# Kernel optimization log

Hardware: AMD Instinct MI355X
Metric: run time of the kernel (lower is better)

Reference implementation:

```python
import jax, jax.numpy as jnp
import numpy as np

PS = 32
D = 256


def setup_inputs() -> dict:
    key = jax.random.key(0)
    ks = jax.random.split(key, 9)
    B, L = 32, 32768
    s_in = 1.0 / np.sqrt(PS)
    s_d = 1.0 / np.sqrt(D)
    return {
        "x": jax.random.normal(ks[0], (B, L), dtype=jnp.float32),
        "W_proj": jax.random.normal(ks[1], (PS, D), dtype=jnp.float32) * s_in,
        "b_proj": jnp.zeros((D,), jnp.float32),
        "W_qkv": jax.random.normal(ks[2], (D, 3 * D), dtype=jnp.float32) * s_d,
        "b_qkv": jnp.zeros((3 * D,), jnp.float32),
        "W_out": jax.random.normal(ks[3], (D, D), dtype=jnp.float32) * s_d,
        "b_out": jnp.zeros((D,), jnp.float32),
        "W_head": jax.random.normal(ks[4], (D, PS), dtype=jnp.float32) * s_d,
        "b_head": jnp.zeros((PS,), jnp.float32),
    }


def reference(x, W_proj, b_proj, W_qkv, b_qkv, W_out, b_out, W_head, b_head):
    B, L = x.shape
    T = L // PS
    # InstanceNorm over full series (torch .std is unbiased -> ddof=1)
    mean = jnp.mean(x, axis=-1, keepdims=True)
    std = jnp.std(x, axis=-1, keepdims=True, ddof=1) + 1e-5
    x_norm = (x - mean) / std
    patches = x_norm.reshape(B, T, PS)
    # Patch embedding
    h = patches @ W_proj + b_proj  # [B, T, D]
    # Single-head causal self-attention (explicit scores, as in source)
    qkv = h @ W_qkv + b_qkv
    q, k, v = jnp.split(qkv, 3, axis=-1)
    scale = 1.0 / jnp.sqrt(jnp.asarray(D, dtype=h.dtype))
    attn = jnp.einsum("btd,bsd->bts", q, k) * scale  # [B, T, T]
    causal = jnp.tril(jnp.ones((T, T), dtype=bool))
    attn = jnp.where(causal, attn, -jnp.inf)
    attn = jax.nn.softmax(attn, axis=-1)
    out = jnp.einsum("bts,bsd->btd", attn, v)
    out = out @ W_out + b_out
    # Prediction head + next-patch MSE loss
    pred = out @ W_head + b_head  # [B, T, PS]
    loss = jnp.mean((pred[:, :-1] - patches[:, 1:]) ** 2)
    return loss
```

## Files before the change

kernel.cpp:

```cpp
#include <hip/hip_runtime.h>
#include <math.h>

#define B_SZ 32
#define L_SZ 32768
#define T_SZ 1024
#define PS_SZ 32
#define D_SZ 256
#define SM_M 10.0f

typedef float f32x4 __attribute__((ext_vector_type(4)));
typedef float f32x16 __attribute__((ext_vector_type(16)));
typedef short s16x8 __attribute__((ext_vector_type(8)));
typedef unsigned short u16x8 __attribute__((ext_vector_type(8)));
typedef unsigned int u32;
typedef unsigned int u32x4 __attribute__((ext_vector_type(4)));

__device__ __forceinline__ unsigned short f2bf(float f) {
  union { float f; unsigned int u; } v; v.f = f;
  unsigned int r = v.u + 0x7FFFu + ((v.u >> 16) & 1u);
  return (unsigned short)(r >> 16);
}

__global__ __launch_bounds__(256) void prep_kernel(const float* __restrict__ x,
                                                   float* __restrict__ sgpart,
                                                   const float* __restrict__ Wp,
                                                   const float* __restrict__ bp,
                                                   const float* __restrict__ Wq,
                                                   const float* __restrict__ bq,
                                                   const float* __restrict__ Wo,
                                                   const float* __restrict__ bo,
                                                   const float* __restrict__ Wh,
                                                   const float* __restrict__ bh,
                                                   float* __restrict__ Wcb,
                                                   unsigned short* __restrict__ WqT,
                                                   unsigned short* __restrict__ WfT,
                                                   float* __restrict__ bfp,
                                                   unsigned int* __restrict__ total,
                                                   float* __restrict__ lsum) {
  __shared__ float red[8];
  const int g = blockIdx.x, tid = threadIdx.x;
  const int w = tid >> 6, lane = tid & 63;
  if (g < 256) {
    const int b = g >> 3;
    const float* p = x + (size_t)b * L_SZ + (size_t)(g & 7) * 4096;
    float s = 0.f, ss = 0.f;
#pragma unroll
    for (int i = 0; i < 4; ++i) {
      float4 f = ((const float4*)p)[tid + i * 256];
      s += f.x + f.y + f.z + f.w;
      ss += f.x * f.x + f.y * f.y + f.z * f.z + f.w * f.w;
    }
#pragma unroll
    for (int off = 32; off >= 1; off >>= 1) {
      s += __shfl_down(s, off);
      ss += __shfl_down(ss, off);
    }
    if (lane == 0) { red[w] = s; red[4 + w] = ss; }
    __syncthreads();
    if (tid == 0) {
      sgpart[g * 2]     = red[0] + red[1] + red[2] + red[3];
      sgpart[g * 2 + 1] = red[4] + red[5] + red[6] + red[7];
    }
  } else if (g < 388) {
    int idx = (g - 256) * 256 + tid;
    if (idx < 33 * 768) {
      int p = idx / 768, j = idx % 768;
      const float* arow = (p < 32) ? (Wp + p * 256) : bp;
      float acc = (p < 32) ? 0.f : bq[j];
      for (int d = 0; d < 256; ++d) acc += arow[d] * Wq[d * 768 + j];
      if (p < 32) WqT[j * 32 + p] = f2bf(acc);
      else Wcb[j] = acc;
    } else {
      int k = idx - 33 * 768;
      if (k < 8192) {
        int p = k >> 8, d = k & 255;
        float acc = 0.f;
        for (int e = 0; e < 256; ++e) acc += Wo[d * 256 + e] * Wh[e * 32 + p];
        WfT[p * 256 + d] = f2bf(acc);
      } else if (k < 8224) {
        int p = k - 8192;
        float acc = bh[p];
        for (int e = 0; e < 256; ++e) acc += bo[e] * Wh[e * 32 + p];
        bfp[p] = acc;
      }
    }
  } else {
    if (tid == 0) { total[0] = 0u; lsum[0] = 0.f; }
  }
}

__global__ __launch_bounds__(256) void qkv_kernel(const float* __restrict__ x,
                                                  const float* __restrict__ sgpart,
                                                  const unsigned short* __restrict__ WqT,
                                                  const float* __restrict__ Wcb,
                                                  unsigned short* __restrict__ Qb,
                                                  unsigned short* __restrict__ Kb,
                                                  unsigned short* __restrict__ Vtt) {
  __shared__ unsigned short T4[4][8448];
  const int tid = threadIdx.x;
  const int w = tid >> 6, lane = tid & 63;
  const int lo = lane & 15, quad = lane >> 4;
  unsigned short* Tw = T4[w];
  const int mbase = blockIdx.x * 128 + w * 32;
  const int b = mbase >> 10;
  float S = 0.f, SS = 0.f;
#pragma unroll
  for (int i = 0; i < 8; ++i) {
    S += sgpart[(b * 8 + i) * 2];
    SS += sgpart[(b * 8 + i) * 2 + 1];
  }
  const float mean = S * (1.f / (float)L_SZ);
  const float var = (SS - S * mean) * (1.f / (float)(L_SZ - 1));
  const float inv = 1.f / (sqrtf(var) + 1e-5f);
  s16x8 af0, af1;
  {
    float4 a = *(const float4*)&x[(size_t)(mbase + lo) * 32 + quad * 8];
    float4 c = *(const float4*)&x[(size_t)(mbase + lo) * 32 + quad * 8 + 4];
    af0[0] = (short)f2bf((a.x - mean) * inv); af0[1] = (short)f2bf((a.y - mean) * inv);
    af0[2] = (short)f2bf((a.z - mean) * inv); af0[3] = (short)f2bf((a.w - mean) * inv);
    af0[4] = (short)f2bf((c.x - mean) * inv); af0[5] = (short)f2bf((c.y - mean) * inv);
    af0[6] = (short)f2bf((c.z - mean) * inv); af0[7] = (short)f2bf((c.w - mean) * inv);
    float4 d = *(const float4*)&x[(size_t)(mbase + 16 + lo) * 32 + quad * 8];
    float4 e = *(const float4*)&x[(size_t)(mbase + 16 + lo) * 32 + quad * 8 + 4];
    af1[0] = (short)f2bf((d.x - mean) * inv); af1[1] = (short)f2bf((d.y - mean) * inv);
    af1[2] = (short)f2bf((d.z - mean) * inv); af1[3] = (short)f2bf((d.w - mean) * inv);
    af1[4] = (short)f2bf((e.x - mean) * inv); af1[5] = (short)f2bf((e.y - mean) * inv);
    af1[6] = (short)f2bf((e.z - mean) * inv); af1[7] = (short)f2bf((e.w - mean) * inv);
  }
#pragma unroll 4
  for (int nt = 0; nt < 16; ++nt) {
    s16x8 bf = *(const s16x8*)&WqT[(size_t)(nt * 16 + lo) * 32 + quad * 8];
    f32x4 c0 = {0.f, 0.f, 0.f, 0.f}, c1 = {0.f, 0.f, 0.f, 0.f};
    c0 = __builtin_amdgcn_mfma_f32_16x16x32_bf16(af0, bf, c0, 0, 0, 0);
    c1 = __builtin_amdgcn_mfma_f32_16x16x32_bf16(af1, bf, c1, 0, 0, 0);
    const int col = nt * 16 + lo;
    const float bi = Wcb[col];
#pragma unroll
    for (int i = 0; i < 4; ++i) {
      Tw[(quad * 4 + i) * 264 + col]      = f2bf((c0[i] + bi) * 0.0625f);
      Tw[(16 + quad * 4 + i) * 264 + col] = f2bf((c1[i] + bi) * 0.0625f);
    }
  }
#pragma unroll
  for (int it = 0; it < 16; ++it) {
    const int gsub = it * 64 + lane;
    const int row = gsub >> 5, c16 = gsub & 31;
    *(u16x8*)&Qb[(size_t)(mbase + row) * 256 + c16 * 8] =
        *(const u16x8*)&Tw[row * 264 + c16 * 8];
  }
#pragma unroll 4
  for (int nt = 0; nt < 16; ++nt) {
    s16x8 bf = *(const s16x8*)&WqT[(size_t)(256 + nt * 16 + lo) * 32 + quad * 8];
    f32x4 c0 = {0.f, 0.f, 0.f, 0.f}, c1 = {0.f, 0.f, 0.f, 0.f};
    c0 = __builtin_amdgcn_mfma_f32_16x16x32_bf16(af0, bf, c0, 0, 0, 0);
    c1 = __builtin_amdgcn_mfma_f32_16x16x32_bf16(af1, bf, c1, 0, 0, 0);
    const int col = nt * 16 + lo;
    const float bi = Wcb[256 + col];
#pragma unroll
    for (int i = 0; i < 4; ++i) {
      Tw[(quad * 4 + i) * 264 + col]      = f2bf(c0[i] + bi);
      Tw[(16 + quad * 4 + i) * 264 + col] = f2bf(c1[i] + bi);
    }
  }
#pragma unroll
  for (int it = 0; it < 16; ++it) {
    const int gsub = it * 64 + lane;
    const int row = gsub >> 5, c16 = gsub & 31;
    *(u16x8*)&Kb[(size_t)(mbase + row) * 256 + c16 * 8] =
        *(const u16x8*)&Tw[row * 264 + c16 * 8];
  }
#pragma unroll 4
  for (int nt2 = 0; nt2 < 16; ++nt2) {
    s16x8 aw = *(const s16x8*)&WqT[(size_t)(512 + nt2 * 16 + lo) * 32 + quad * 8];
    f32x4 c0 = {0.f, 0.f, 0.f, 0.f}, c1 = {0.f, 0.f, 0.f, 0.f};
    c0 = __builtin_amdgcn_mfma_f32_16x16x32_bf16(aw, af0, c0, 0, 0, 0);
    c1 = __builtin_amdgcn_mfma_f32_16x16x32_bf16(aw, af1, c1, 0, 0, 0);
#pragma unroll
    for (int i = 0; i < 4; ++i) {
      const int d = nt2 * 16 + quad * 4 + i;
      const float bv = Wcb[512 + d];
      Tw[d * 32 + lo]      = f2bf(c0[i] + bv);
      Tw[d * 32 + 16 + lo] = f2bf(c1[i] + bv);
    }
  }
  {
    const int ktq = (mbase >> 5) & 31;
    const size_t vb = ((size_t)b * 32 + ktq) * 8192;
#pragma unroll
    for (int it = 0; it < 16; ++it) {
      const int gsub = it * 64 + lane;
      *(u16x8*)&Vtt[vb + gsub * 8] = *(const u16x8*)&Tw[gsub * 8];
    }
  }
}

__global__ __launch_bounds__(256, 2) void attn_kernel(const unsigned short* __restrict__ Qb,
                                                      const unsigned short* __restrict__ Kb,
                                                      const unsigned short* __restrict__ Vtt,
                                                      const unsigned short* __restrict__ WfT,
                                                      const float* __restrict__ bfp,
                                                      const float* __restrict__ x,
                                                      const float* __restrict__ sgpart,
                                                      float* __restrict__ lsum,
                                                      unsigned int* __restrict__ total,
                                                      float* __restrict__ out) {
  __shared__ float CO0[8192];
  __shared__ float CO1[8192];
  __shared__ float OlL[4][32];
  __shared__ unsigned int flagv;
  const int g = blockIdx.x;
  const int b = (g & 7) * 4 + ((g >> 3) & 3);
  const int p = g >> 5;
  const int tid = threadIdx.x;
  const int w = tid >> 6, lane = tid & 63;
  const int cl = lane & 31, hi = lane >> 5;

  const unsigned short* KbB = Kb + (size_t)b * 262144;
  const unsigned short* VtB = Vtt + (size_t)b * 262144;

  float S_ = 0.f, SS = 0.f;
#pragma unroll
  for (int i = 0; i < 8; ++i) {
    S_ += sgpart[(b * 8 + i) * 2];
    SS += sgpart[(b * 8 + i) * 2 + 1];
  }
  const float mean = S_ * (1.f / (float)L_SZ);
  const float var = (SS - S_ * mean) * (1.f / (float)(L_SZ - 1));
  const float invb = 1.f / (sqrtf(var) + 1e-5f);
  float lacc = 0.f;

#pragma unroll 1
  for (int half = 0; half < 2; ++half) {
    const int ti = half ? (31 - p) : p;
    const int qr0 = ti * 32;

    s16x8 qf[16];
    {
      const size_t qrow = ((size_t)b * 1024 + qr0 + cl) * 256;
#pragma unroll
      for (int cb = 0; cb < 16; ++cb)
        qf[cb] = *(const s16x8*)&Qb[qrow + cb * 16 + hi * 8];
    }

    f32x16 O[8];
#pragma unroll
    for (int dt = 0; dt < 8; ++dt)
#pragma unroll
      for (int i = 0; i < 16; ++i) O[dt][i] = 0.f;
    float Ol = 0.f;

    for (int kt = w; kt <= ti; kt += 4) {
      const unsigned short* kp = KbB + (size_t)kt * 8192 + cl * 256 + hi * 8;
      f32x16 Sx;
#pragma unroll
      for (int i = 0; i < 16; ++i) Sx[i] = 0.f;
#pragma unroll
      for (int cb = 0; cb < 16; ++cb) {
        s16x8 kf = *(const s16x8*)&kp[cb * 16];
        Sx = __builtin_amdgcn_mfma_f32_32x32x16_bf16(kf, qf[cb], Sx, 0, 0, 0);
      }
      float e[16];
      const bool diag = (kt == ti);
#pragma unroll
      for (int r = 0; r < 16; ++r) {
        const int trow = (r & 3) + 8 * (r >> 2) + 4 * hi;
        float ev = __expf(Sx[r] - SM_M);
        if (diag && trow > cl) ev = 0.f;
        e[r] = ev;
        Ol += ev;
      }
      u32 w8[8];
#pragma unroll
      for (int m = 0; m < 8; ++m)
        w8[m] = (u32)f2bf(e[2 * m]) | ((u32)f2bf(e[2 * m + 1]) << 16);
      const u32 r1 = (u32)__shfl_xor((int)(hi ? w8[0] : w8[2]), 32);
      const u32 r2 = (u32)__shfl_xor((int)(hi ? w8[1] : w8[3]), 32);
      const u32 r3 = (u32)__shfl_xor((int)(hi ? w8[4] : w8[6]), 32);
      const u32 r4 = (u32)__shfl_xor((int)(hi ? w8[5] : w8[7]), 32);
      union { u32x4 u; s16x8 s; } p0, p1;
      p0.u[0] = hi ? r1 : w8[0];
      p0.u[1] = hi ? r2 : w8[1];
      p0.u[2] = hi ? w8[2] : r1;
      p0.u[3] = hi ? w8[3] : r2;
      p1.u[0] = hi ? r3 : w8[4];
      p1.u[1] = hi ? r4 : w8[5];
      p1.u[2] = hi ? w8[6] : r3;
      p1.u[3] = hi ? w8[7] : r4;
      const unsigned short* vp = VtB + (size_t)kt * 8192 + cl * 32 + hi * 8;
#pragma unroll
      for (int dt = 0; dt < 8; ++dt) {
        s16x8 v0 = *(const s16x8*)&vp[dt * 1024];
        s16x8 v1 = *(const s16x8*)&vp[dt * 1024 + 16];
        O[dt] = __builtin_amdgcn_mfma_f32_32x32x16_bf16(p0.s, v0, O[dt], 0, 0, 0);
        O[dt] = __builtin_amdgcn_mfma_f32_32x32x16_bf16(p1.s, v1, O[dt], 0, 0, 0);
      }
    }
    Ol += __shfl_xor(Ol, 32);

    __syncthreads();
    if (w == 1) {
#pragma unroll
      for (int dt = 0; dt < 8; ++dt)
#pragma unroll
        for (int r = 0; r < 16; ++r) {
          const int row = (r & 3) + 8 * (r >> 2) + 4 * hi;
          CO0[row * 256 + dt * 32 + cl] = O[dt][r];
        }
    }
    if (w == 3) {
#pragma unroll
      for (int dt = 0; dt < 8; ++dt)
#pragma unroll
        for (int r = 0; r < 16; ++r) {
          const int row = (r & 3) + 8 * (r >> 2) + 4 * hi;
          CO1[row * 256 + dt * 32 + cl] = O[dt][r];
        }
    }
    if (hi == 0) OlL[w][cl] = Ol;
    __syncthreads();
    if (w == 0) {
#pragma unroll
      for (int dt = 0; dt < 8; ++dt)
#pragma unroll
        for (int r = 0; r < 16; ++r) {
          const int row = (r & 3) + 8 * (r >> 2) + 4 * hi;
          O[dt][r] += CO0[row * 256 + dt * 32 + cl];
        }
    }
    if (w == 2) {
#pragma unroll
      for (int dt = 0; dt < 8; ++dt)
#pragma unroll
        for (int r = 0; r < 16; ++r) {
          const int row = (r & 3) + 8 * (r >> 2) + 4 * hi;
          O[dt][r] += CO1[row * 256 + dt * 32 + cl];
        }
    }
    __syncthreads();
    if (w == 2) {
#pragma unroll
      for (int dt = 0; dt < 8; ++dt)
#pragma unroll
        for (int r = 0; r < 16; ++r) {
          const int row = (r & 3) + 8 * (r >> 2) + 4 * hi;
          CO0[row * 256 + dt * 32 + cl] = O[dt][r];
        }
    }
    __syncthreads();
    if (w == 0) {
#pragma unroll
      for (int dt = 0; dt < 8; ++dt)
#pragma unroll
        for (int r = 0; r < 16; ++r) {
          const int row = (r & 3) + 8 * (r >> 2) + 4 * hi;
          O[dt][r] += CO0[row * 256 + dt * 32 + cl];
        }
      float ivr[16];
#pragma unroll
      for (int r = 0; r < 16; ++r) {
        const int row = (r & 3) + 8 * (r >> 2) + 4 * hi;
        ivr[r] = 1.f / (OlL[0][row] + OlL[1][row] + OlL[2][row] + OlL[3][row]);
      }
      unsigned short* OLw = (unsigned short*)CO0;
#pragma unroll
      for (int dt = 0; dt < 8; ++dt)
#pragma unroll
        for (int r = 0; r < 16; ++r) {
          const int row = (r & 3) + 8 * (r >> 2) + 4 * hi;
          OLw[row * 264 + dt * 32 + cl] = f2bf(O[dt][r] * ivr[r]);
        }
      s16x8 af[16];
#pragma unroll
      for (int cb = 0; cb < 16; ++cb)
        af[cb] = *(const s16x8*)&OLw[cl * 264 + cb * 16 + hi * 8];
      f32x16 hacc;
#pragma unroll
      for (int i = 0; i < 16; ++i) hacc[i] = 0.f;
#pragma unroll
      for (int cb = 0; cb < 16; ++cb) {
        s16x8 bfr = *(const s16x8*)&WfT[(size_t)cl * 256 + cb * 16 + hi * 8];
        hacc = __builtin_amdgcn_mfma_f32_32x32x16_bf16(af[cb], bfr, hacc, 0, 0, 0);
      }
      const float ba = bfp[cl];
#pragma unroll
      for (int r = 0; r < 16; ++r) {
        const int row = (r & 3) + 8 * (r >> 2) + 4 * hi;
        const int t = qr0 + row;
        if (t < 1023) {
          const float pr = hacc[r] + ba;
          const float tg = (x[(size_t)b * L_SZ + (t + 1) * 32 + cl] - mean) * invb;
          const float d = pr - tg;
          lacc += d * d;
        }
      }
    }
  }

#pragma unroll
  for (int off = 32; off >= 1; off >>= 1) lacc += __shfl_down(lacc, off);
  if (tid == 0) {
    atomicAdd(lsum, lacc);
    __threadfence();
    unsigned int prev = atomicAdd(total, 1u);
    flagv = (prev == 511u) ? 1u : 0u;
  }
  __syncthreads();
  if (flagv && tid == 0) {
    float tot = atomicAdd(lsum, 0.0f);
    out[0] = tot * (1.f / (float)(B_SZ * (T_SZ - 1) * PS_SZ));
  }
}

extern "C" void kernel_launch(void* const* d_in, const int* in_sizes, int n_in,
                              void* d_out, int out_size, void* d_ws, size_t ws_size,
                              hipStream_t stream) {
  const float* x      = (const float*)d_in[0];
  const float* W_proj = (const float*)d_in[1];
  const float* b_proj = (const float*)d_in[2];
  const float* W_qkv  = (const float*)d_in[3];
  const float* b_qkv  = (const float*)d_in[4];
  const float* W_out  = (const float*)d_in[5];
  const float* b_out  = (const float*)d_in[6];
  const float* W_head = (const float*)d_in[7];
  const float* b_head = (const float*)d_in[8];
  float* out = (float*)d_out;
  char* ws = (char*)d_ws;

  unsigned short* Qb     = (unsigned short*)ws;
  unsigned short* Kb     = (unsigned short*)(ws + (16ull << 20));
  unsigned short* Vtt    = (unsigned short*)(ws + (32ull << 20));
  char* tail = ws + (48ull << 20);
  float*          Wcb    = (float*)tail;
  unsigned short* WqT    = (unsigned short*)(tail + 4096);
  unsigned short* WfT    = (unsigned short*)(tail + 65536);
  float*          bfp    = (float*)(tail + 98304);
  float*          sgpart = (float*)(tail + 102400);
  unsigned int*   total  = (unsigned int*)(tail + 106496);
  float*          lsum   = (float*)(tail + 106496 + 64);

  prep_kernel<<<389, 256, 0, stream>>>(x, sgpart, W_proj, b_proj, W_qkv, b_qkv,
                                       W_out, b_out, W_head, b_head,
                                       Wcb, WqT, WfT, bfp, total, lsum);
  qkv_kernel<<<256, 256, 0, stream>>>(x, sgpart, WqT, Wcb, Qb, Kb, Vtt);
  attn_kernel<<<512, 256, 0, stream>>>(Qb, Kb, Vtt, WfT, bfp, x, sgpart, lsum, total, out);
}
```

Baseline: 196.9 us.

## Split attention work across waves by key parity and head-dim half

The four waves are now arranged as a 2x2 grid. Each wave covers every other key tile (kp) and only half of the 256 value columns (dh), instead of every fourth key tile across all columns. This halves the O accumulator registers per wave and shrinks the cross-wave reduction to one shared-memory exchange, with the normalization and bf16 packing done in parallel by two waves. In exchange, each wave recomputes the QK^T scores and softmax for its key tiles twice as often, which doubles the score MFMA and exp work.

```diff
diff --git a/kernel.cpp b/kernel.cpp
--- a/kernel.cpp
+++ b/kernel.cpp
@@ -204,8 +204,9 @@
                                                       float* __restrict__ lsum,
                                                       unsigned int* __restrict__ total,
                                                       float* __restrict__ out) {
-  __shared__ float CO0[8192];
-  __shared__ float CO1[8192];
+  __shared__ float CO0[4096];
+  __shared__ float CO1[4096];
+  __shared__ unsigned short OLs[8448];
   __shared__ float OlL[4][32];
   __shared__ unsigned int flagv;
   const int g = blockIdx.x;
@@ -213,6 +214,7 @@
   const int p = g >> 5;
   const int tid = threadIdx.x;
   const int w = tid >> 6, lane = tid & 63;
+  const int kp = w & 1, dh = w >> 1;
   const int cl = lane & 31, hi = lane >> 5;
 
   const unsigned short* KbB = Kb + (size_t)b * 262144;
@@ -242,21 +244,21 @@
         qf[cb] = *(const s16x8*)&Qb[qrow + cb * 16 + hi * 8];
     }
 
-    f32x16 O[8];
-#pragma unroll
-    for (int dt = 0; dt < 8; ++dt)
-#pragma unroll
-      for (int i = 0; i < 16; ++i) O[dt][i] = 0.f;
+    f32x16 O[4];
+#pragma unroll
+    for (int i4 = 0; i4 < 4; ++i4)
+#pragma unroll
+      for (int i = 0; i < 16; ++i) O[i4][i] = 0.f;
     float Ol = 0.f;
 
-    for (int kt = w; kt <= ti; kt += 4) {
-      const unsigned short* kp = KbB + (size_t)kt * 8192 + cl * 256 + hi * 8;
+    for (int kt = kp; kt <= ti; kt += 2) {
+      const unsigned short* kp_ = KbB + (size_t)kt * 8192 + cl * 256 + hi * 8;
       f32x16 Sx;
 #pragma unroll
       for (int i = 0; i < 16; ++i) Sx[i] = 0.f;
 #pragma unroll
       for (int cb = 0; cb < 16; ++cb) {
-        s16x8 kf = *(const s16x8*)&kp[cb * 16];
+        s16x8 kf = *(const s16x8*)&kp_[cb * 16];
         Sx = __builtin_amdgcn_mfma_f32_32x32x16_bf16(kf, qf[cb], Sx, 0, 0, 0);
       }
       float e[16];
@@ -286,13 +288,13 @@
       p1.u[1] = hi ? r4 : w8[5];
       p1.u[2] = hi ? w8[6] : r3;
       p1.u[3] = hi ? w8[7] : r4;
-      const unsigned short* vp = VtB + (size_t)kt * 8192 + cl * 32 + hi * 8;
-#pragma unroll
-      for (int dt = 0; dt < 8; ++dt) {
-        s16x8 v0 = *(const s16x8*)&vp[dt * 1024];
-        s16x8 v1 = *(const s16x8*)&vp[dt * 1024 + 16];
-        O[dt] = __builtin_amdgcn_mfma_f32_32x32x16_bf16(p0.s, v0, O[dt], 0, 0, 0);
-        O[dt] = __builtin_amdgcn_mfma_f32_32x32x16_bf16(p1.s, v1, O[dt], 0, 0, 0);
+      const unsigned short* vp = VtB + (size_t)kt * 8192 + (dh * 4) * 1024 + cl * 32 + hi * 8;
+#pragma unroll
+      for (int i4 = 0; i4 < 4; ++i4) {
+        s16x8 v0 = *(const s16x8*)&vp[i4 * 1024];
+        s16x8 v1 = *(const s16x8*)&vp[i4 * 1024 + 16];
+        O[i4] = __builtin_amdgcn_mfma_f32_32x32x16_bf16(p0.s, v0, O[i4], 0, 0, 0);
+        O[i4] = __builtin_amdgcn_mfma_f32_32x32x16_bf16(p1.s, v1, O[i4], 0, 0, 0);
       }
     }
     Ol += __shfl_xor(Ol, 32);
@@ -300,79 +302,47 @@
     __syncthreads();
     if (w == 1) {
 #pragma unroll
-      for (int dt = 0; dt < 8; ++dt)
+      for (int i4 = 0; i4 < 4; ++i4)
 #pragma unroll
         for (int r = 0; r < 16; ++r) {
           const int row = (r & 3) + 8 * (r >> 2) + 4 * hi;
-          CO0[row * 256 + dt * 32 + cl] = O[dt][r];
+          CO0[row * 128 + i4 * 32 + cl] = O[i4][r];
         }
     }
     if (w == 3) {
 #pragma unroll
-      for (int dt = 0; dt < 8; ++dt)
+      for (int i4 = 0; i4 < 4; ++i4)
 #pragma unroll
         for (int r = 0; r < 16; ++r) {
           const int row = (r & 3) + 8 * (r >> 2) + 4 * hi;
-          CO1[row * 256 + dt * 32 + cl] = O[dt][r];
+          CO1[row * 128 + i4 * 32 + cl] = O[i4][r];
         }
     }
     if (hi == 0) OlL[w][cl] = Ol;
     __syncthreads();
-    if (w == 0) {
-#pragma unroll
-      for (int dt = 0; dt < 8; ++dt)
+    if (kp == 0) {
+      const float* CO = dh ? CO1 : CO0;
+      float ivr[16];
+#pragma unroll
+      for (int r = 0; r < 16; ++r) {
+        const int row = (r & 3) + 8 * (r >> 2) + 4 * hi;
+        ivr[r] = 1.f / (OlL[0][row] + OlL[1][row]);
+      }
+#pragma unroll
+      for (int i4 = 0; i4 < 4; ++i4)
 #pragma unroll
         for (int r = 0; r < 16; ++r) {
           const int row = (r & 3) + 8 * (r >> 2) + 4 * hi;
-          O[dt][r] += CO0[row * 256 + dt * 32 + cl];
-        }
-    }
-    if (w == 2) {
-#pragma unroll
-      for (int dt = 0; dt < 8; ++dt)
-#pragma unroll
-        for (int r = 0; r < 16; ++r) {
-          const int row = (r & 3) + 8 * (r >> 2) + 4 * hi;
-          O[dt][r] += CO1[row * 256 + dt * 32 + cl];
-        }
-    }
-    __syncthreads();
-    if (w == 2) {
-#pragma unroll
-      for (int dt = 0; dt < 8; ++dt)
-#pragma unroll
-        for (int r = 0; r < 16; ++r) {
-          const int row = (r & 3) + 8 * (r >> 2) + 4 * hi;
-          CO0[row * 256 + dt * 32 + cl] = O[dt][r];
+          const float ov = O[i4][r] + CO[row * 128 + i4 * 32 + cl];
+          OLs[row * 264 + (dh * 4 + i4) * 32 + cl] = f2bf(ov * ivr[r]);
         }
     }
     __syncthreads();
     if (w == 0) {
-#pragma unroll
-      for (int dt = 0; dt < 8; ++dt)
-#pragma unroll
-        for (int r = 0; r < 16; ++r) {
-          const int row = (r & 3) + 8 * (r >> 2) + 4 * hi;
-          O[dt][r] += CO0[row * 256 + dt * 32 + cl];
-        }
-      float ivr[16];
-#pragma unroll
-      for (int r = 0; r < 16; ++r) {
-        const int row = (r & 3) + 8 * (r >> 2) + 4 * hi;
-        ivr[r] = 1.f / (OlL[0][row] + OlL[1][row] + OlL[2][row] + OlL[3][row]);
-      }
-      unsigned short* OLw = (unsigned short*)CO0;
-#pragma unroll
-      for (int dt = 0; dt < 8; ++dt)
-#pragma unroll
-        for (int r = 0; r < 16; ++r) {
-          const int row = (r & 3) + 8 * (r >> 2) + 4 * hi;
-          OLw[row * 264 + dt * 32 + cl] = f2bf(O[dt][r] * ivr[r]);
-        }
       s16x8 af[16];
 #pragma unroll
       for (int cb = 0; cb < 16; ++cb)
-        af[cb] = *(const s16x8*)&OLw[cl * 264 + cb * 16 + hi * 8];
+        af[cb] = *(const s16x8*)&OLs[cl * 264 + cb * 16 + hi * 8];
       f32x16 hacc;
 #pragma unroll
       for (int i = 0; i < 16; ++i) hacc[i] = 0.f;
```

Result: slower. 211.7 us (+7.5%).
